# Optimization experiments

Measured on AMD Instinct MI355X. Metric: run time of the kernel, lower is better.

The kernel has to match this reference:

```python
import jax, jax.numpy as jnp
import numpy as np

B, S, F, O = 128, 8, 32, 16  # batch, board_size, in_features, out_features
D = 2 * S - 1                # diff_size = 15 relative offsets per axis


def setup_inputs() -> dict:
    key = jax.random.key(0)
    k1, k2, k3 = jax.random.split(key, 3)
    inp = jax.random.normal(k1, (B, S, S, F), dtype=jnp.float32)
    # torch.nn.Bilinear init: U(-1/sqrt(in1_features), 1/sqrt(in1_features))
    bound = 1.0 / np.sqrt(F)
    W = jax.random.uniform(k2, (D, D, O, F, F), jnp.float32, -bound, bound)
    b = jax.random.uniform(k3, (D, D, O), jnp.float32, -bound, bound)
    return {"inp": inp, "W": W, "b": b}


def reference(inp, W, b):
    # inp: (B, S, S, F); W: (D, D, O, F, F); b: (D, D, O)
    s = inp.shape[1]
    idx = jnp.arange(s)
    # offset index: off[a, bb] = bb - a + (s - 1), in [0, 2s-2]
    off = idx[None, :] - idx[:, None] + (s - 1)  # (S, S)
    # gather per-pair bilinear weights: Wg[ax, bx, ay, by] = W[bx-ax+7, by-ay+7]
    Wg = W[off[:, :, None, None], off[None, None, :, :]]  # (S,S,S,S,O,F,F)
    bg = b[off[:, :, None, None], off[None, None, :, :]]  # (S,S,S,S,O) [ax,bx,ay,by]
    # out[b, ax, ay, bx, by, o] = a_i W_oij b_j + bias_o
    out = jnp.einsum('bxyi,xXyYoij,bXYj->bxyXYo', inp, Wg, inp)
    out = out + bg.transpose(0, 2, 1, 3, 4)[None]  # bias to [ax,ay,bx,by,o]
    return out
```

## Files before the change

### kernel.cpp

```cpp
#include <hip/hip_runtime.h>

typedef _Float16 f16;
typedef _Float16 f16x8 __attribute__((ext_vector_type(8)));
typedef float f32x4 __attribute__((ext_vector_type(4)));
typedef unsigned int u32;
typedef const __attribute__((address_space(1))) u32* gas1_t;
typedef __attribute__((address_space(3))) u32* las3_t;

#define WGRAN 460800
#define IGRAN 32768

__global__ __launch_bounds__(256) void convert_kernel(
    const float* __restrict__ W, const float* __restrict__ inp,
    f16* __restrict__ W_h, f16* __restrict__ inp_h)
{
    const int g = blockIdx.x * 256 + threadIdx.x;
    if (g < WGRAN) {
        const int dxdy = g >> 11;
        const int r = g & 2047;
        const int i = r >> 6, o = (r >> 2) & 15, quad = r & 3;
        const float* src = W + (size_t)dxdy * 16384 + o * 1024 + i * 32 + quad * 8;
        const float4 v0 = *(const float4*)src;
        const float4 v1 = *(const float4*)(src + 4);
        f16x8 h = { (f16)v0.x, (f16)v0.y, (f16)v0.z, (f16)v0.w,
                    (f16)v1.x, (f16)v1.y, (f16)v1.z, (f16)v1.w };
        *(f16x8*)(W_h + (size_t)g * 8) = h;
    } else {
        const int k = g - WGRAN;
        const float* src = inp + (size_t)k * 8;
        const float4 v0 = *(const float4*)src;
        const float4 v1 = *(const float4*)(src + 4);
        f16x8 h = { (f16)v0.x, (f16)v0.y, (f16)v0.z, (f16)v0.w,
                    (f16)v1.x, (f16)v1.y, (f16)v1.z, (f16)v1.w };
        *(f16x8*)(inp_h + (size_t)k * 8) = h;
    }
}

__global__ __launch_bounds__(256, 2) void rel_mfma4(
    const f16* __restrict__ W_h,
    const f16* __restrict__ inp_h,
    const float* __restrict__ bias,
    float* __restrict__ out)
{
    extern __shared__ __align__(16) f16 Wl[];

    const int hw = blockIdx.x;
    const int X = hw & 7, y = (hw >> 3) & 7, x = (hw >> 6) & 7;
    const int dx = X - x + 7;

    const int t = threadIdx.x;
    const int lane = t & 63;
    const int wave = t >> 6;
    const int quad = lane >> 4;
    const int m = lane & 15;

    const f16* wbase = W_h + (size_t)(dx * 15 + 7 - y) * 16384;

    #pragma unroll
    for (int it = 0; it < 8; ++it) {
        const int idx = (it * 256 + t) * 8;
        __builtin_amdgcn_global_load_lds((gas1_t)(wbase + idx),
                                         (las3_t)&Wl[idx], 16, 0, 0);
    }

    f16x8 a0[4], a1[4], c0[8], c1[8];
    const int b0 = wave * 32 + m;
    const int b1 = b0 + 16;
    {
        const f16* ar0 = inp_h + ((b0 * 8 + x) * 8 + y) * 32;
        const f16* ar1 = inp_h + ((b1 * 8 + x) * 8 + y) * 32;
        #pragma unroll
        for (int g = 0; g < 4; ++g) {
            a0[g] = *(const f16x8*)(ar0 + g * 8);
            a1[g] = *(const f16x8*)(ar1 + g * 8);
        }
        const f16* cr0 = inp_h + (b0 * 8 + X) * 256 + quad * 8;
        const f16* cr1 = inp_h + (b1 * 8 + X) * 256 + quad * 8;
        #pragma unroll
        for (int Yi = 0; Yi < 8; ++Yi) {
            c0[Yi] = *(const f16x8*)(cr0 + Yi * 32);
            c1[Yi] = *(const f16x8*)(cr1 + Yi * 32);
        }
    }

    __syncthreads();

    const int bid_base = ((x * 8 + y) * 8 + X) * 8;

    #pragma unroll
    for (int Y = 0; Y < 8; ++Y) {
        const int cur = Y & 1;

        if (Y < 7) {
            const f16* nbase = wbase + (size_t)(Y + 1) * 16384;
            f16* ldst = Wl + (cur ^ 1) * 16384;
            #pragma unroll
            for (int it = 0; it < 8; ++it) {
                const int idx = (it * 256 + t) * 8;
                __builtin_amdgcn_global_load_lds((gas1_t)(nbase + idx),
                                                 (las3_t)&ldst[idx], 16, 0, 0);
            }
        }

        f32x4 acc0 = {0.f, 0.f, 0.f, 0.f};
        f32x4 acc1 = {0.f, 0.f, 0.f, 0.f};
        const f16* wl = Wl + cur * 16384 + m * 32 + quad * 8;
        f16x8 bfrag = *(const f16x8*)(wl);
        #pragma unroll
        for (int kb = 0; kb < 32; ++kb) {
            const f16x8 bcur = bfrag;
            if (kb < 31)
                bfrag = *(const f16x8*)(wl + (kb + 1) * 512);
            const f16 av0 = a0[kb >> 3][kb & 7];
            const f16 av1 = a1[kb >> 3][kb & 7];
            const f16x8 af0 = c0[Y] * av0;
            const f16x8 af1 = c1[Y] * av1;
            acc0 = __builtin_amdgcn_mfma_f32_16x16x32_f16(af0, bcur, acc0, 0, 0, 0);
            acc1 = __builtin_amdgcn_mfma_f32_16x16x32_f16(af1, bcur, acc1, 0, 0, 0);
        }

        const int dxdy = dx * 15 + (Y - y + 7);
        const int bid = bid_base + Y;
        const float bv = bias[dxdy * 16 + m];
        #pragma unroll
        for (int r = 0; r < 4; ++r) {
            const int bb = wave * 32 + quad * 4 + r;
            out[((size_t)bb * 4096 + bid) * 16 + m]        = acc0[r] + bv;
            out[((size_t)(bb + 16) * 4096 + bid) * 16 + m] = acc1[r] + bv;
        }

        __syncthreads();
    }
}

extern "C" void kernel_launch(void* const* d_in, const int* in_sizes, int n_in,
                              void* d_out, int out_size, void* d_ws, size_t ws_size,
                              hipStream_t stream)
{
    const float* inp  = (const float*)d_in[0];
    const float* W    = (const float*)d_in[1];
    const float* bias = (const float*)d_in[2];
    float* out = (float*)d_out;

    f16* W_h   = (f16*)d_ws;
    f16* inp_h = (f16*)d_ws + (size_t)WGRAN * 8;

    hipLaunchKernelGGL(convert_kernel, dim3((WGRAN + IGRAN) / 256), dim3(256), 0,
                       stream, W, inp, W_h, inp_h);
    hipLaunchKernelGGL(rel_mfma4, dim3(512), dim3(256), 65536, stream,
                       W_h, inp_h, bias, out);
}
```

Measured before the change: 105.8 us.

## Halve block to two waves, each handling four batch tiles per weight fragment

The MFMA kernel now runs 128 threads per block with each wave covering 64 batch rows (four 16-row tiles), so every LDS weight fragment feeds four MFMAs instead of two. The per-Y input fragments are double-buffered from global memory instead of holding all eight in registers, and the LDS weight fragment prefetch depth grows to four. This cuts LDS reads per MFMA and raises register-level reuse. In exchange there are half as many waves per block, with launch bounds now set to one block per SM, which may reduce latency hiding and occupancy.

```diff
diff --git a/kernel.cpp b/kernel.cpp
--- a/kernel.cpp
+++ b/kernel.cpp
@@ -36,7 +36,7 @@
     }
 }
 
-__global__ __launch_bounds__(256, 2) void rel_mfma4(
+__global__ __launch_bounds__(128, 1) void rel_mfma5(
     const f16* __restrict__ W_h,
     const f16* __restrict__ inp_h,
     const float* __restrict__ bias,
@@ -50,38 +50,34 @@
 
     const int t = threadIdx.x;
     const int lane = t & 63;
-    const int wave = t >> 6;
+    const int w = t >> 6;
     const int quad = lane >> 4;
     const int m = lane & 15;
 
     const f16* wbase = W_h + (size_t)(dx * 15 + 7 - y) * 16384;
 
     #pragma unroll
-    for (int it = 0; it < 8; ++it) {
-        const int idx = (it * 256 + t) * 8;
+    for (int it = 0; it < 16; ++it) {
+        const int idx = (it * 128 + t) * 8;
         __builtin_amdgcn_global_load_lds((gas1_t)(wbase + idx),
                                          (las3_t)&Wl[idx], 16, 0, 0);
     }
 
-    f16x8 a0[4], a1[4], c0[8], c1[8];
-    const int b0 = wave * 32 + m;
-    const int b1 = b0 + 16;
-    {
-        const f16* ar0 = inp_h + ((b0 * 8 + x) * 8 + y) * 32;
-        const f16* ar1 = inp_h + ((b1 * 8 + x) * 8 + y) * 32;
+    f16x8 a[4][4];
+    int brow[4];
+    #pragma unroll
+    for (int n = 0; n < 4; ++n) {
+        brow[n] = w * 64 + n * 16 + m;
+        const f16* ar = inp_h + ((brow[n] * 8 + x) * 8 + y) * 32;
         #pragma unroll
-        for (int g = 0; g < 4; ++g) {
-            a0[g] = *(const f16x8*)(ar0 + g * 8);
-            a1[g] = *(const f16x8*)(ar1 + g * 8);
-        }
-        const f16* cr0 = inp_h + (b0 * 8 + X) * 256 + quad * 8;
-        const f16* cr1 = inp_h + (b1 * 8 + X) * 256 + quad * 8;
-        #pragma unroll
-        for (int Yi = 0; Yi < 8; ++Yi) {
-            c0[Yi] = *(const f16x8*)(cr0 + Yi * 32);
-            c1[Yi] = *(const f16x8*)(cr1 + Yi * 32);
-        }
+        for (int g = 0; g < 4; ++g) a[n][g] = *(const f16x8*)(ar + g * 8);
     }
+
+    f16x8 cc[2][4];
+    #pragma unroll
+    for (int n = 0; n < 4; ++n)
+        cc[0][n] = *(const f16x8*)(inp_h + ((brow[n] * 8 + X) * 8 + 0) * 32
+                                   + quad * 8);
 
     __syncthreads();
 
@@ -95,38 +91,50 @@
             const f16* nbase = wbase + (size_t)(Y + 1) * 16384;
             f16* ldst = Wl + (cur ^ 1) * 16384;
             #pragma unroll
-            for (int it = 0; it < 8; ++it) {
-                const int idx = (it * 256 + t) * 8;
+            for (int it = 0; it < 16; ++it) {
+                const int idx = (it * 128 + t) * 8;
                 __builtin_amdgcn_global_load_lds((gas1_t)(nbase + idx),
                                                  (las3_t)&ldst[idx], 16, 0, 0);
             }
+            #pragma unroll
+            for (int n = 0; n < 4; ++n)
+                cc[cur ^ 1][n] = *(const f16x8*)(inp_h
+                    + ((brow[n] * 8 + X) * 8 + (Y + 1)) * 32 + quad * 8);
+        }
+        const int dxdy = dx * 15 + (Y - y + 7);
+        const float bv = bias[dxdy * 16 + m];
+
+        f32x4 acc[4];
+        #pragma unroll
+        for (int n = 0; n < 4; ++n) acc[n] = (f32x4){0.f, 0.f, 0.f, 0.f};
+
+        const f16* wl = Wl + cur * 16384 + m * 32 + quad * 8;
+        f16x8 bf[4];
+        #pragma unroll
+        for (int p = 0; p < 4; ++p) bf[p] = *(const f16x8*)(wl + p * 512);
+
+        #pragma unroll
+        for (int kb = 0; kb < 32; ++kb) {
+            const f16x8 bcur = bf[kb & 3];
+            if (kb < 28)
+                bf[kb & 3] = *(const f16x8*)(wl + (kb + 4) * 512);
+            #pragma unroll
+            for (int n = 0; n < 4; ++n) {
+                const f16 av = a[n][kb >> 3][kb & 7];
+                const f16x8 af = cc[cur][n] * av;
+                acc[n] = __builtin_amdgcn_mfma_f32_16x16x32_f16(af, bcur,
+                                                                acc[n], 0, 0, 0);
+            }
         }
 
-        f32x4 acc0 = {0.f, 0.f, 0.f, 0.f};
-        f32x4 acc1 = {0.f, 0.f, 0.f, 0.f};
-        const f16* wl = Wl + cur * 16384 + m * 32 + quad * 8;
-        f16x8 bfrag = *(const f16x8*)(wl);
+        const int bid = bid_base + Y;
         #pragma unroll
-        for (int kb = 0; kb < 32; ++kb) {
-            const f16x8 bcur = bfrag;
-            if (kb < 31)
-                bfrag = *(const f16x8*)(wl + (kb + 1) * 512);
-            const f16 av0 = a0[kb >> 3][kb & 7];
-            const f16 av1 = a1[kb >> 3][kb & 7];
-            const f16x8 af0 = c0[Y] * av0;
-            const f16x8 af1 = c1[Y] * av1;
-            acc0 = __builtin_amdgcn_mfma_f32_16x16x32_f16(af0, bcur, acc0, 0, 0, 0);
-            acc1 = __builtin_amdgcn_mfma_f32_16x16x32_f16(af1, bcur, acc1, 0, 0, 0);
-        }
-
-        const int dxdy = dx * 15 + (Y - y + 7);
-        const int bid = bid_base + Y;
-        const float bv = bias[dxdy * 16 + m];
-        #pragma unroll
-        for (int r = 0; r < 4; ++r) {
-            const int bb = wave * 32 + quad * 4 + r;
-            out[((size_t)bb * 4096 + bid) * 16 + m]        = acc0[r] + bv;
-            out[((size_t)(bb + 16) * 4096 + bid) * 16 + m] = acc1[r] + bv;
+        for (int n = 0; n < 4; ++n) {
+            #pragma unroll
+            for (int r = 0; r < 4; ++r) {
+                const int b = w * 64 + n * 16 + quad * 4 + r;
+                out[((size_t)b * 4096 + bid) * 16 + m] = acc[n][r] + bv;
+            }
         }
 
         __syncthreads();
@@ -147,6 +155,6 @@
 
     hipLaunchKernelGGL(convert_kernel, dim3((WGRAN + IGRAN) / 256), dim3(256), 0,
                        stream, W, inp, W_h, inp_h);
-    hipLaunchKernelGGL(rel_mfma4, dim3(512), dim3(256), 65536, stream,
+    hipLaunchKernelGGL(rel_mfma5, dim3(512), dim3(128), 65536, stream,
                        W_h, inp_h, bias, out);
 }
```

New measurement: 114.7 us. 1.08x slower.
